# Kernel optimization log

Hardware: AMD Instinct MI355X
Metric: run time of the kernel (lower is better)

## Reference

```python
import jax, jax.numpy as jnp
import numpy as np

# Config: num_elems=64, num_attrs=8, vocab=1024, max_len=16, hidden=1024,
# input_embedding_dim=64, output_embedding_dim=256, num_layers=1, LSTM cell,
# attention=False, peeky=False, message=None, eval mode (argmax sampling).
B, A, NE = 2048, 8, 64
EIN, EOUT, H, V, L = 64, 256, 1024, 1024, 16


def setup_inputs() -> dict:
    key = jax.random.key(0)
    ks = jax.random.split(key, 12)
    s = 0.05
    return {
        "x": jax.random.randint(ks[0], (B, A), 0, NE),
        "in_emb": jax.random.normal(ks[1], (NE, EIN), jnp.float32) * s,
        "out_emb": jax.random.normal(ks[2], (V, EOUT), jnp.float32) * s,
        "W_in": jax.random.normal(ks[3], (H, A * EIN), jnp.float32) * s,
        "b_in": jnp.zeros((H,), jnp.float32),
        "W_ih": jax.random.normal(ks[4], (4 * H, EOUT), jnp.float32) * s,
        "b_ih": jnp.zeros((4 * H,), jnp.float32),
        "W_hh": jax.random.normal(ks[5], (4 * H, H), jnp.float32) * s,
        "b_hh": jnp.zeros((4 * H,), jnp.float32),
        "W_out": jax.random.normal(ks[6], (V, H), jnp.float32) * s,
        "b_out": jnp.zeros((V,), jnp.float32),
        "sos": jax.random.normal(ks[7], (EOUT,), jnp.float32),
    }


def reference(x, in_emb, out_emb, W_in, b_in, W_ih, b_ih, W_hh, b_hh, W_out, b_out, sos):
    bsz = x.shape[0]
    # input embedding -> concat attrs -> initial hidden
    ie = in_emb[x].reshape(bsz, -1)              # [B, A*EIN]
    h0 = ie @ W_in.T + b_in                      # [B, H]
    c0 = jnp.zeros_like(h0)                      # LSTM cell state starts at 0
    emb0 = jnp.broadcast_to(sos, (bsz, sos.shape[0]))  # SOS embedding [B, EOUT]

    def step(carry, _):
        h, c, emb = carry
        gates = emb @ W_ih.T + b_ih + h @ W_hh.T + b_hh  # [B, 4H], torch gate order i,f,g,o
        i, f, g, o = jnp.split(gates, 4, axis=-1)
        c_new = jax.nn.sigmoid(f) * c + jax.nn.sigmoid(i) * jnp.tanh(g)
        h_new = jax.nn.sigmoid(o) * jnp.tanh(c_new)
        logits = h_new @ W_out.T + b_out                 # [B, V]
        symbol = jnp.argmax(logits, axis=-1)             # eval-mode greedy sampling
        return (h_new, c_new, out_emb[symbol]), (symbol, logits)

    _, (syms, logits) = jax.lax.scan(step, (h0, c0, emb0), None, length=L)
    sequence = syms.T                                    # [B, L]
    logits = jnp.transpose(logits, (1, 0, 2))            # [B, L, V]
    return sequence, logits
```

## Files before the change

### kernel.cpp

```cpp
#include <hip/hip_runtime.h>
#include <math.h>

constexpr int kB    = 2048;
constexpr int kA    = 8;
constexpr int kEin  = 64;
constexpr int kEout = 256;
constexpr int kH    = 1024;
constexpr int kV    = 1024;
constexpr int kL    = 16;
constexpr int kKin  = kA * kEin;
constexpr int kNG   = 4 * kH;
constexpr float kInvLo = 1.0f / 2048.0f;

using half8 = __attribute__((ext_vector_type(8))) _Float16;
using half4 = __attribute__((ext_vector_type(4))) _Float16;
using f32x4 = __attribute__((ext_vector_type(4))) float;

#define GLL16(g, l) __builtin_amdgcn_global_load_lds(                        \
    (const __attribute__((address_space(1))) void*)(g),                      \
    (__attribute__((address_space(3))) void*)(l), 16, 0, 0)

__device__ __forceinline__ float sigm(float x) { return 1.0f / (1.0f + expf(-x)); }

struct HL { _Float16 hi, lo; };
__device__ __forceinline__ HL split2v(float x) {
  HL r;
  r.hi = (_Float16)x;
  r.lo = (_Float16)((x - (float)r.hi) * 2048.0f);
  return r;
}

__device__ __forceinline__ size_t packA(int m, int k) {
  return ((((size_t)(m >> 7) * 32 + (k >> 5)) * 4 + ((k >> 3) & 3)) * 128 + (m & 127)) * 8 + (k & 7);
}

__global__ __launch_bounds__(256) void init_state(float* __restrict__ c,
                                                  int* __restrict__ sym) {
  int i = blockIdx.x * 256 + threadIdx.x;
  c[i] = 0.0f;
  if (i < kB) sym[i] = kV;
}

__global__ __launch_bounds__(256) void split_plain(const float* __restrict__ src,
                                                   _Float16* __restrict__ hi,
                                                   _Float16* __restrict__ lo,
                                                   int n4) {
  int i = blockIdx.x * 256 + threadIdx.x;
  if (i >= n4) return;
  float4 v = ((const float4*)src)[i];
  half4 h, l;
  HL s0 = split2v(v.x), s1 = split2v(v.y), s2 = split2v(v.z), s3 = split2v(v.w);
  h.x = s0.hi; l.x = s0.lo; h.y = s1.hi; l.y = s1.lo;
  h.z = s2.hi; l.z = s2.lo; h.w = s3.hi; l.w = s3.lo;
  *(half4*)(hi + (size_t)i * 4) = h;
  *(half4*)(lo + (size_t)i * 4) = l;
}

__global__ __launch_bounds__(320) void split_gates_w(const float* __restrict__ W_ih,
                                                     const float* __restrict__ W_hh,
                                                     _Float16* __restrict__ rm_hi,
                                                     _Float16* __restrict__ rm_lo,
                                                     _Float16* __restrict__ p_hi,
                                                     _Float16* __restrict__ p_lo) {
  const int n  = blockIdx.x;
  const int k4 = threadIdx.x * 4;
  const int g  = (n >> 4) & 3;
  const int j  = ((n >> 6) << 4) | (n & 15);
  const int src = g * kH + j;
  float4 v = (k4 < kEout) ? *(const float4*)&W_ih[(size_t)src * kEout + k4]
                          : *(const float4*)&W_hh[(size_t)src * kH + (k4 - kEout)];
  half4 h, l;
  HL s0 = split2v(v.x), s1 = split2v(v.y), s2 = split2v(v.z), s3 = split2v(v.w);
  h.x = s0.hi; l.x = s0.lo; h.y = s1.hi; l.y = s1.lo;
  h.z = s2.hi; l.z = s2.lo; h.w = s3.hi; l.w = s3.lo;
  if (k4 < kEout) {
    *(half4*)(rm_hi + (size_t)n * kEout + k4) = h;
    *(half4*)(rm_lo + (size_t)n * kEout + k4) = l;
  } else {
    const int kp = k4 - kEout;
    const size_t ad = packA(n, kp);
    *(half4*)(p_hi + ad) = h;
    *(half4*)(p_lo + ad) = l;
  }
}

__global__ __launch_bounds__(256) void split_pack_wo(const float* __restrict__ W_out,
                                                     _Float16* __restrict__ hi,
                                                     _Float16* __restrict__ lo) {
  const int n  = blockIdx.x;
  const int k4 = threadIdx.x * 4;
  float4 v = *(const float4*)&W_out[(size_t)n * kH + k4];
  half4 h, l;
  HL s0 = split2v(v.x), s1 = split2v(v.y), s2 = split2v(v.z), s3 = split2v(v.w);
  h.x = s0.hi; l.x = s0.lo; h.y = s1.hi; l.y = s1.lo;
  h.z = s2.hi; l.z = s2.lo; h.w = s3.hi; l.w = s3.lo;
  const size_t ad = ((((size_t)(n >> 5) * 32 + (k4 >> 5)) * 4 + ((k4 >> 3) & 3)) * 32
                     + (n & 31)) * 8 + (k4 & 7);
  *(half4*)(hi + ad) = h;
  *(half4*)(lo + ad) = l;
}

__global__ __launch_bounds__(256) void h0_gemm(const int* __restrict__ x,
                                               const float* __restrict__ in_emb,
                                               const float* __restrict__ W_in,
                                               const float* __restrict__ b_in,
                                               _Float16* __restrict__ h_hi,
                                               _Float16* __restrict__ h_lo) {
  __shared__ float As[16][128];
  __shared__ float Bs[16][128];
  const int t  = threadIdx.x;
  const int tx = t & 15, ty = t >> 4;
  const int r  = t >> 1;
  const int kc = (t & 1) * 8;
  const int m0 = blockIdx.x * 128;
  const int n0 = blockIdx.y * 128;
  float acc[8][8] = {};
  for (int k0 = 0; k0 < kKin; k0 += 16) {
    const int kk   = k0 + kc;
    const int attr = kk >> 6;
    const int e    = kk & 63;
    const int idx  = x[(m0 + r) * kA + attr];
    const float* pa = in_emb + (size_t)idx * kEin + e;
    float4 a0 = *(const float4*)pa;
    float4 a1 = *(const float4*)(pa + 4);
    const float* pb = W_in + (size_t)(n0 + r) * kKin + kk;
    float4 b0 = *(const float4*)pb;
    float4 b1 = *(const float4*)(pb + 4);
    __syncthreads();
    As[kc+0][r]=a0.x; As[kc+1][r]=a0.y; As[kc+2][r]=a0.z; As[kc+3][r]=a0.w;
    As[kc+4][r]=a1.x; As[kc+5][r]=a1.y; As[kc+6][r]=a1.z; As[kc+7][r]=a1.w;
    Bs[kc+0][r]=b0.x; Bs[kc+1][r]=b0.y; Bs[kc+2][r]=b0.z; Bs[kc+3][r]=b0.w;
    Bs[kc+4][r]=b1.x; Bs[kc+5][r]=b1.y; Bs[kc+6][r]=b1.z; Bs[kc+7][r]=b1.w;
    __syncthreads();
#pragma unroll
    for (int k = 0; k < 16; ++k) {
      float a[8], b[8];
      *(float4*)&a[0] = *(const float4*)&As[k][ty*8];
      *(float4*)&a[4] = *(const float4*)&As[k][ty*8+4];
      *(float4*)&b[0] = *(const float4*)&Bs[k][tx*8];
      *(float4*)&b[4] = *(const float4*)&Bs[k][tx*8+4];
#pragma unroll
      for (int i = 0; i < 8; ++i)
#pragma unroll
        for (int j = 0; j < 8; ++j)
          acc[i][j] = fmaf(a[i], b[j], acc[i][j]);
    }
  }
#pragma unroll
  for (int i = 0; i < 8; ++i) {
    const int gm  = m0 + ty*8 + i;
    const int gn0 = n0 + tx*8;
    half8 h8, l8;
#pragma unroll
    for (int j = 0; j < 8; ++j) {
      HL s = split2v(acc[i][j] + b_in[gn0 + j]);
      h8[j] = s.hi; l8[j] = s.lo;
    }
    const size_t ad = packA(gm, gn0);
    *(half8*)(h_hi + ad) = h8;
    *(half8*)(h_lo + ad) = l8;
  }
}

__global__ __launch_bounds__(256, 2) void eg_gemm(
    const _Float16* __restrict__ oe_hi, const _Float16* __restrict__ oe_lo,
    const _Float16* __restrict__ Wg_hi, const _Float16* __restrict__ Wg_lo,
    float* __restrict__ Eg) {
  __shared__ __align__(16) _Float16 Ah[4][128][8], Al[4][128][8],
                                    Bh[4][128][8], Bl[4][128][8];
  const int t    = threadIdx.x;
  const int m0   = blockIdx.x * 128;
  const int by   = blockIdx.y;
  const int n0   = by * 128;
  const int r    = t & 127, q = t >> 7;
  const int rw   = r & 64;
  const int lane = t & 63, wid = t >> 6;
  const int wm   = (wid >> 1) * 64;
  const int wnv  = wid & 1;
  const int lc   = lane & 15, lg = lane >> 4;
  f32x4 acc1[4][4] = {}; f32x4 acc2[4][4] = {};
  for (int k0 = 0; k0 < kEout; k0 += 32) {
    const size_t oa = (size_t)(m0 + r) * kEout + k0 + q * 16;
    const size_t ob = (size_t)(n0 + r) * kEout + k0 + q * 16;
    __syncthreads();
    GLL16(oe_hi + oa,     &Ah[2*q  ][rw][0]);
    GLL16(oe_hi + oa + 8, &Ah[2*q+1][rw][0]);
    GLL16(oe_lo + oa,     &Al[2*q  ][rw][0]);
    GLL16(oe_lo + oa + 8, &Al[2*q+1][rw][0]);
    GLL16(Wg_hi + ob,     &Bh[2*q  ][rw][0]);
    GLL16(Wg_hi + ob + 8, &Bh[2*q+1][rw][0]);
    GLL16(Wg_lo + ob,     &Bl[2*q  ][rw][0]);
    GLL16(Wg_lo + ob + 8, &Bl[2*q+1][rw][0]);
    __syncthreads();
    half8 ah[4], al[4], bh[4], bl[4];
#pragma unroll
    for (int mf = 0; mf < 4; ++mf) {
      ah[mf] = *(const half8*)&Ah[lg][wm + mf*16 + lc][0];
      al[mf] = *(const half8*)&Al[lg][wm + mf*16 + lc][0];
    }
#pragma unroll
    for (int nf = 0; nf < 4; ++nf) {
      bh[nf] = *(const half8*)&Bh[lg][wnv*64 + nf*16 + lc][0];
      bl[nf] = *(const half8*)&Bl[lg][wnv*64 + nf*16 + lc][0];
    }
#pragma unroll
    for (int mf = 0; mf < 4; ++mf)
#pragma unroll
      for (int nf = 0; nf < 4; ++nf) {
        acc1[mf][nf] = __builtin_amdgcn_mfma_f32_16x16x32_f16(ah[mf], bh[nf], acc1[mf][nf], 0, 0, 0);
        acc2[mf][nf] = __builtin_amdgcn_mfma_f32_16x16x32_f16(ah[mf], bl[nf], acc2[mf][nf], 0, 0, 0);
        acc2[mf][nf] = __builtin_amdgcn_mfma_f32_16x16x32_f16(al[mf], bh[nf], acc2[mf][nf], 0, 0, 0);
      }
  }
#pragma unroll
  for (int mf = 0; mf < 4; ++mf)
#pragma unroll
    for (int reg = 0; reg < 4; ++reg) {
      const int m = m0 + wm + mf * 16 + lg * 4 + reg;
#pragma unroll
      for (int nf = 0; nf < 4; ++nf)
        Eg[(size_t)m * kNG + n0 + wnv*64 + nf*16 + lc] =
            acc1[mf][nf][reg] + acc2[mf][nf][reg] * kInvLo;
    }
}

__global__ __launch_bounds__(256) void gs_row(const float* __restrict__ sos,
                                              const float* __restrict__ W_ih,
                                              float* __restrict__ Eg) {
  const int n = blockIdx.x * 256 + threadIdx.x;
  const int g = (n >> 4) & 3;
  const int j = ((n >> 6) << 4) | (n & 15);
  const float* w = W_ih + (size_t)(g * kH + j) * kEout;
  float s = 0.0f;
#pragma unroll 4
  for (int k = 0; k < kEout; k += 4) {
    float4 wv = *(const float4*)&w[k];
    float4 sv = *(const float4*)&sos[k];
    s += wv.x*sv.x + wv.y*sv.y + wv.z*sv.z + wv.w*sv.w;
  }
  Eg[(size_t)kV * kNG + n] = s;
}

__global__ __launch_bounds__(256, 2) void gates_lstm_mfma(
    const _Float16* __restrict__ hp_hi,  const _Float16* __restrict__ hp_lo,
    const _Float16* __restrict__ Wgp_hi, const _Float16* __restrict__ Wgp_lo,
    const float* __restrict__ Eg,        const int* __restrict__ sym,
    const float* __restrict__ b_ih, const float* __restrict__ b_hh,
    float* __restrict__ c,
    _Float16* __restrict__ ho_hi, _Float16* __restrict__ ho_lo) {
  const int t    = threadIdx.x;
  const int bx   = blockIdx.x;
  const int by   = blockIdx.y;
  const int m0   = bx * 128;
  const int lane = t & 63, wid = t >> 6;
  const int wm   = (wid >> 1) * 64;
  const int wnv  = wid & 1;
  const int lc   = lane & 15, lg = lane >> 4;
  constexpr int SK = 4 * 128 * 8;

  size_t adr_a = (size_t)bx * 32 * SK + ((size_t)lg * 128 + wm + lc) * 8;
  size_t adr_b = (size_t)by * 32 * SK + ((size_t)lg * 128 + wnv * 64 + lc) * 8;

  f32x4 acc1[4][4] = {}; f32x4 acc2[4][4] = {};
  for (int ks = 0; ks < 32; ++ks) {
    half8 ah[4], al[4], bh[4], bl[4];
#pragma unroll
    for (int mf = 0; mf < 4; ++mf) {
      ah[mf] = *(const half8*)(hp_hi + adr_a + mf * 128);
      al[mf] = *(const half8*)(hp_lo + adr_a + mf * 128);
    }
#pragma unroll
    for (int nf = 0; nf < 4; ++nf) {
      bh[nf] = *(const half8*)(Wgp_hi + adr_b + nf * 128);
      bl[nf] = *(const half8*)(Wgp_lo + adr_b + nf * 128);
    }
#pragma unroll
    for (int mf = 0; mf < 4; ++mf)
#pragma unroll
      for (int nf = 0; nf < 4; ++nf) {
        acc1[mf][nf] = __builtin_amdgcn_mfma_f32_16x16x32_f16(ah[mf], bh[nf], acc1[mf][nf], 0, 0, 0);
        acc2[mf][nf] = __builtin_amdgcn_mfma_f32_16x16x32_f16(ah[mf], bl[nf], acc2[mf][nf], 0, 0, 0);
        acc2[mf][nf] = __builtin_amdgcn_mfma_f32_16x16x32_f16(al[mf], bh[nf], acc2[mf][nf], 0, 0, 0);
      }
    adr_a += SK; adr_b += SK;
  }
  const int j   = by * 32 + wnv * 16 + lc;
  const int nbase = by * 128 + wnv * 64 + lc;
  const int jks = j >> 5, jq = (j >> 3) & 3, je = j & 7;
  float bb[4];
#pragma unroll
  for (int nf = 0; nf < 4; ++nf) bb[nf] = b_ih[nf * kH + j] + b_hh[nf * kH + j];
#pragma unroll
  for (int mf = 0; mf < 4; ++mf)
#pragma unroll
    for (int reg = 0; reg < 4; ++reg) {
      const int lr = wm + mf * 16 + lg * 4 + reg;
      const int m  = m0 + lr;
      const size_t off = (size_t)m * kH + j;
      const float* Erow = Eg + (size_t)sym[m] * kNG + nbase;
      const float vi = acc1[mf][0][reg] + acc2[mf][0][reg] * kInvLo + bb[0] + Erow[0];
      const float vf = acc1[mf][1][reg] + acc2[mf][1][reg] * kInvLo + bb[1] + Erow[16];
      const float vg = acc1[mf][2][reg] + acc2[mf][2][reg] * kInvLo + bb[2] + Erow[32];
      const float vo = acc1[mf][3][reg] + acc2[mf][3][reg] * kInvLo + bb[3] + Erow[48];
      const float cn = sigm(vf) * c[off] + sigm(vi) * tanhf(vg);
      const float hn = sigm(vo) * tanhf(cn);
      c[off] = cn;
      HL s = split2v(hn);
      const size_t ad = ((((size_t)bx * 32 + jks) * 4 + jq) * 128 + lr) * 8 + je;
      ho_hi[ad] = s.hi; ho_lo[ad] = s.lo;
    }
}

__global__ __launch_bounds__(256, 2) void logits_mfma(
    const _Float16* __restrict__ hp_hi, const _Float16* __restrict__ hp_lo,
    const _Float16* __restrict__ Wop_hi, const _Float16* __restrict__ Wop_lo,
    const float* __restrict__ b_out, float* __restrict__ out) {
  const int t    = threadIdx.x;
  const int bx   = blockIdx.x;
  const int by   = blockIdx.y;
  const int lane = t & 63, wid = t >> 6;
  const int wm   = wid * 32;
  const int lc   = lane & 15, lg = lane >> 4;
  constexpr int SKA = 4 * 128 * 8;
  constexpr int SKB = 4 * 32 * 8;

  size_t adr_a = (size_t)bx * 32 * SKA + ((size_t)lg * 128 + wm + lc) * 8;
  size_t adr_b = (size_t)by * 32 * SKB + ((size_t)lg * 32 + lc) * 8;

  f32x4 acc1[2][2] = {}; f32x4 acc2[2][2] = {};
#pragma unroll 2
  for (int ks = 0; ks < 32; ++ks) {
    half8 ah[2], al[2], bh[2], bl[2];
#pragma unroll
    for (int mf = 0; mf < 2; ++mf) {
      ah[mf] = *(const half8*)(hp_hi + adr_a + mf * 128);
      al[mf] = *(const half8*)(hp_lo + adr_a + mf * 128);
    }
#pragma unroll
    for (int nf = 0; nf < 2; ++nf) {
      bh[nf] = *(const half8*)(Wop_hi + adr_b + nf * 128);
      bl[nf] = *(const half8*)(Wop_lo + adr_b + nf * 128);
    }
#pragma unroll
    for (int mf = 0; mf < 2; ++mf)
#pragma unroll
      for (int nf = 0; nf < 2; ++nf) {
        acc1[mf][nf] = __builtin_amdgcn_mfma_f32_16x16x32_f16(ah[mf], bh[nf], acc1[mf][nf], 0, 0, 0);
        acc2[mf][nf] = __builtin_amdgcn_mfma_f32_16x16x32_f16(ah[mf], bl[nf], acc2[mf][nf], 0, 0, 0);
        acc2[mf][nf] = __builtin_amdgcn_mfma_f32_16x16x32_f16(al[mf], bh[nf], acc2[mf][nf], 0, 0, 0);
      }
    adr_a += SKA; adr_b += SKB;
  }
#pragma unroll
  for (int mf = 0; mf < 2; ++mf)
#pragma unroll
    for (int reg = 0; reg < 4; ++reg) {
      const int m = bx * 128 + wm + mf * 16 + lg * 4 + reg;
#pragma unroll
      for (int nf = 0; nf < 2; ++nf) {
        const int n = by * 32 + nf * 16 + lc;
        out[(size_t)m * (kL * kV) + n] = acc1[mf][nf][reg] + acc2[mf][nf][reg] * kInvLo + b_out[n];
      }
    }
}

__global__ __launch_bounds__(256) void argmax_gather(const float* __restrict__ logits_t,
                                                     float* __restrict__ seq,
                                                     int* __restrict__ sym,
                                                     int t) {
  const int lane = threadIdx.x & 63;
  const int wv   = threadIdx.x >> 6;
  const int b    = blockIdx.x * 4 + wv;
  const float* row = logits_t + (size_t)b * (kL * kV);
  float m = -3.4e38f;
  int  mi = 0;
#pragma unroll
  for (int jr = 0; jr < kV / 64; ++jr) {
    const int idx = jr * 64 + lane;
    const float v = row[idx];
    if (v > m) { m = v; mi = idx; }
  }
#pragma unroll
  for (int off = 32; off > 0; off >>= 1) {
    const float om = __shfl_down(m, off);
    const int   oi = __shfl_down(mi, off);
    if (om > m || (om == m && oi < mi)) { m = om; mi = oi; }
  }
  if (lane == 0) {
    seq[(size_t)b * kL + t] = (float)mi;
    sym[b] = mi;
  }
}

extern "C" void kernel_launch(void* const* d_in, const int* in_sizes, int n_in,
                              void* d_out, int out_size, void* d_ws, size_t ws_size,
                              hipStream_t stream) {
  const int*   x       = (const int*)d_in[0];
  const float* in_emb  = (const float*)d_in[1];
  const float* out_emb = (const float*)d_in[2];
  const float* W_in    = (const float*)d_in[3];
  const float* b_in    = (const float*)d_in[4];
  const float* W_ih    = (const float*)d_in[5];
  const float* b_ih    = (const float*)d_in[6];
  const float* W_hh    = (const float*)d_in[7];
  const float* b_hh    = (const float*)d_in[8];
  const float* W_out   = (const float*)d_in[9];
  const float* b_out   = (const float*)d_in[10];
  const float* sos     = (const float*)d_in[11];

  float* cb  = (float*)d_ws;
  float* Eg  = cb + (size_t)kB * kH;
  int*   sym = (int*)(Eg + (size_t)(kV + 1) * kNG);
  _Float16* hp = (_Float16*)(sym + kB);
  const size_t nBH = (size_t)kB * kH;
  _Float16* hA_hi  = hp;            _Float16* hA_lo  = hp + nBH;
  _Float16* hB_hi  = hp + 2*nBH;    _Float16* hB_lo  = hp + 3*nBH;
  _Float16* Wgrm_hi = hp + 4*nBH;
  _Float16* Wgrm_lo = Wgrm_hi + (size_t)kNG*kEout;
  _Float16* Wgp_hi  = Wgrm_lo + (size_t)kNG*kEout;
  _Float16* Wgp_lo  = Wgp_hi + (size_t)kNG*kH;
  _Float16* Wop_hi  = Wgp_lo + (size_t)kNG*kH;
  _Float16* Wop_lo  = Wop_hi + (size_t)kV*kH;
  _Float16* oe_hi   = Wop_lo + (size_t)kV*kH;
  _Float16* oe_lo   = oe_hi + (size_t)kV*kEout;

  float* seq    = (float*)d_out;
  float* logits = seq + (size_t)kB * kL;

  init_state<<<(kB * kH) / 256, 256, 0, stream>>>(cb, sym);
  split_gates_w<<<kNG, 320, 0, stream>>>(W_ih, W_hh, Wgrm_hi, Wgrm_lo, Wgp_hi, Wgp_lo);
  split_pack_wo<<<kV, 256, 0, stream>>>(W_out, Wop_hi, Wop_lo);
  split_plain<<<(kV * kEout / 4) / 256, 256, 0, stream>>>(out_emb, oe_hi, oe_lo, kV * kEout / 4);
  eg_gemm<<<dim3(kV / 128, kNG / 128), 256, 0, stream>>>(oe_hi, oe_lo, Wgrm_hi, Wgrm_lo, Eg);
  gs_row<<<kNG / 256, 256, 0, stream>>>(sos, W_ih, Eg);
  h0_gemm<<<dim3(kB / 128, kH / 128), 256, 0, stream>>>(x, in_emb, W_in, b_in, hA_hi, hA_lo);

  for (int t = 0; t < kL; ++t) {
    const _Float16* hi_h = (t & 1) ? hB_hi : hA_hi;
    const _Float16* hi_l = (t & 1) ? hB_lo : hA_lo;
    _Float16* ho_h = (t & 1) ? hA_hi : hB_hi;
    _Float16* ho_l = (t & 1) ? hA_lo : hB_lo;
    gates_lstm_mfma<<<dim3(kB / 128, kNG / 128), 256, 0, stream>>>(
        hi_h, hi_l, Wgp_hi, Wgp_lo, Eg, sym, b_ih, b_hh, cb, ho_h, ho_l);
    logits_mfma<<<dim3(kB / 128, kV / 32), 256, 0, stream>>>(
        ho_h, ho_l, Wop_hi, Wop_lo, b_out, logits + (size_t)t * kV);
    argmax_gather<<<kB / 4, 256, 0, stream>>>(logits + (size_t)t * kV, seq, sym, t);
  }
}
```

Measured before the change: 1.813 ms.

## Fuse argmax into logits GEMM via atomic keys; move h0 GEMM to MFMA

The separate argmax kernel is removed. Each logits block reduces its 32 columns and atomically maxes a packed 64-bit (value, index) key into a per-step key array, and the next gates kernel decodes the symbol and writes the sequence entry. The fp32 h0 GEMM is replaced by prepacked split-fp16 operands and an MFMA kernel. This saves one launch per step and a re-read of the logits, at the cost of global 64-bit atomics and extra packing kernels.

```diff
diff --git a/kernel.cpp b/kernel.cpp
--- a/kernel.cpp
+++ b/kernel.cpp
@@ -15,6 +15,7 @@
 using half8 = __attribute__((ext_vector_type(8))) _Float16;
 using half4 = __attribute__((ext_vector_type(4))) _Float16;
 using f32x4 = __attribute__((ext_vector_type(4))) float;
+using u64   = unsigned long long;
 
 #define GLL16(g, l) __builtin_amdgcn_global_load_lds(                        \
     (const __attribute__((address_space(1))) void*)(g),                      \
@@ -30,15 +31,24 @@
   return r;
 }
 
-__device__ __forceinline__ size_t packA(int m, int k) {
-  return ((((size_t)(m >> 7) * 32 + (k >> 5)) * 4 + ((k >> 3) & 3)) * 128 + (m & 127)) * 8 + (k & 7);
+__device__ __forceinline__ size_t packAK(int m, int k, int nks) {
+  return ((((size_t)(m >> 7) * nks + (k >> 5)) * 4 + ((k >> 3) & 3)) * 128 + (m & 127)) * 8 + (k & 7);
+}
+
+__device__ __forceinline__ u64 amax_key(float v, int idx) {
+  unsigned b = __float_as_uint(v);
+  unsigned u = (b & 0x80000000u) ? ~b : (b | 0x80000000u);
+  return ((u64)u << 10) | (unsigned)(1023 - idx);
+}
+__device__ __forceinline__ int key_sym(u64 k) {
+  return k == 0 ? kV : 1023 - (int)(k & 1023);
 }
 
 __global__ __launch_bounds__(256) void init_state(float* __restrict__ c,
-                                                  int* __restrict__ sym) {
+                                                  u64* __restrict__ keys) {
   int i = blockIdx.x * 256 + threadIdx.x;
   c[i] = 0.0f;
-  if (i < kB) sym[i] = kV;
+  if (i < 17 * kB) keys[i] = 0ull;
 }
 
 __global__ __launch_bounds__(256) void split_plain(const float* __restrict__ src,
@@ -77,8 +87,7 @@
     *(half4*)(rm_hi + (size_t)n * kEout + k4) = h;
     *(half4*)(rm_lo + (size_t)n * kEout + k4) = l;
   } else {
-    const int kp = k4 - kEout;
-    const size_t ad = packA(n, kp);
+    const size_t ad = packAK(n, k4 - kEout, 32);
     *(half4*)(p_hi + ad) = h;
     *(half4*)(p_lo + ad) = l;
   }
@@ -100,66 +109,91 @@
   *(half4*)(lo + ad) = l;
 }
 
-__global__ __launch_bounds__(256) void h0_gemm(const int* __restrict__ x,
+__global__ __launch_bounds__(128) void pack_a0(const int* __restrict__ x,
                                                const float* __restrict__ in_emb,
-                                               const float* __restrict__ W_in,
-                                               const float* __restrict__ b_in,
-                                               _Float16* __restrict__ h_hi,
-                                               _Float16* __restrict__ h_lo) {
-  __shared__ float As[16][128];
-  __shared__ float Bs[16][128];
-  const int t  = threadIdx.x;
-  const int tx = t & 15, ty = t >> 4;
-  const int r  = t >> 1;
-  const int kc = (t & 1) * 8;
-  const int m0 = blockIdx.x * 128;
-  const int n0 = blockIdx.y * 128;
-  float acc[8][8] = {};
-  for (int k0 = 0; k0 < kKin; k0 += 16) {
-    const int kk   = k0 + kc;
-    const int attr = kk >> 6;
-    const int e    = kk & 63;
-    const int idx  = x[(m0 + r) * kA + attr];
-    const float* pa = in_emb + (size_t)idx * kEin + e;
-    float4 a0 = *(const float4*)pa;
-    float4 a1 = *(const float4*)(pa + 4);
-    const float* pb = W_in + (size_t)(n0 + r) * kKin + kk;
-    float4 b0 = *(const float4*)pb;
-    float4 b1 = *(const float4*)(pb + 4);
-    __syncthreads();
-    As[kc+0][r]=a0.x; As[kc+1][r]=a0.y; As[kc+2][r]=a0.z; As[kc+3][r]=a0.w;
-    As[kc+4][r]=a1.x; As[kc+5][r]=a1.y; As[kc+6][r]=a1.z; As[kc+7][r]=a1.w;
-    Bs[kc+0][r]=b0.x; Bs[kc+1][r]=b0.y; Bs[kc+2][r]=b0.z; Bs[kc+3][r]=b0.w;
-    Bs[kc+4][r]=b1.x; Bs[kc+5][r]=b1.y; Bs[kc+6][r]=b1.z; Bs[kc+7][r]=b1.w;
-    __syncthreads();
-#pragma unroll
-    for (int k = 0; k < 16; ++k) {
-      float a[8], b[8];
-      *(float4*)&a[0] = *(const float4*)&As[k][ty*8];
-      *(float4*)&a[4] = *(const float4*)&As[k][ty*8+4];
-      *(float4*)&b[0] = *(const float4*)&Bs[k][tx*8];
-      *(float4*)&b[4] = *(const float4*)&Bs[k][tx*8+4];
-#pragma unroll
-      for (int i = 0; i < 8; ++i)
-#pragma unroll
-        for (int j = 0; j < 8; ++j)
-          acc[i][j] = fmaf(a[i], b[j], acc[i][j]);
-    }
-  }
-#pragma unroll
-  for (int i = 0; i < 8; ++i) {
-    const int gm  = m0 + ty*8 + i;
-    const int gn0 = n0 + tx*8;
-    half8 h8, l8;
-#pragma unroll
-    for (int j = 0; j < 8; ++j) {
-      HL s = split2v(acc[i][j] + b_in[gn0 + j]);
-      h8[j] = s.hi; l8[j] = s.lo;
-    }
-    const size_t ad = packA(gm, gn0);
-    *(half8*)(h_hi + ad) = h8;
-    *(half8*)(h_lo + ad) = l8;
-  }
+                                               _Float16* __restrict__ hi,
+                                               _Float16* __restrict__ lo) {
+  const int m  = blockIdx.x;
+  const int k4 = threadIdx.x * 4;
+  const int idx = x[m * kA + (k4 >> 6)];
+  float4 v = *(const float4*)&in_emb[(size_t)idx * kEin + (k4 & 63)];
+  half4 h, l;
+  HL s0 = split2v(v.x), s1 = split2v(v.y), s2 = split2v(v.z), s3 = split2v(v.w);
+  h.x = s0.hi; l.x = s0.lo; h.y = s1.hi; l.y = s1.lo;
+  h.z = s2.hi; l.z = s2.lo; h.w = s3.hi; l.w = s3.lo;
+  const size_t ad = packAK(m, k4, 16);
+  *(half4*)(hi + ad) = h;
+  *(half4*)(lo + ad) = l;
+}
+
+__global__ __launch_bounds__(128) void pack_w0(const float* __restrict__ W_in,
+                                               _Float16* __restrict__ hi,
+                                               _Float16* __restrict__ lo) {
+  const int n  = blockIdx.x;
+  const int k4 = threadIdx.x * 4;
+  float4 v = *(const float4*)&W_in[(size_t)n * kKin + k4];
+  half4 h, l;
+  HL s0 = split2v(v.x), s1 = split2v(v.y), s2 = split2v(v.z), s3 = split2v(v.w);
+  h.x = s0.hi; l.x = s0.lo; h.y = s1.hi; l.y = s1.lo;
+  h.z = s2.hi; l.z = s2.lo; h.w = s3.hi; l.w = s3.lo;
+  const size_t ad = packAK(n, k4, 16);
+  *(half4*)(hi + ad) = h;
+  *(half4*)(lo + ad) = l;
+}
+
+__global__ __launch_bounds__(256, 2) void h0_mfma(
+    const _Float16* __restrict__ a_hi, const _Float16* __restrict__ a_lo,
+    const _Float16* __restrict__ w_hi, const _Float16* __restrict__ w_lo,
+    const float* __restrict__ b_in,
+    _Float16* __restrict__ h_hi, _Float16* __restrict__ h_lo) {
+  const int t    = threadIdx.x;
+  const int bx   = blockIdx.x;
+  const int by   = blockIdx.y;
+  const int lane = t & 63, wid = t >> 6;
+  const int wm   = (wid >> 1) * 64;
+  const int wnv  = wid & 1;
+  const int lc   = lane & 15, lg = lane >> 4;
+  constexpr int SK = 4 * 128 * 8;
+
+  size_t adr_a = (size_t)bx * 16 * SK + ((size_t)lg * 128 + wm + lc) * 8;
+  size_t adr_b = (size_t)by * 16 * SK + ((size_t)lg * 128 + wnv * 64 + lc) * 8;
+
+  f32x4 acc1[4][4] = {}; f32x4 acc2[4][4] = {};
+  for (int ks = 0; ks < 16; ++ks) {
+    half8 ah[4], al[4], bh[4], bl[4];
+#pragma unroll
+    for (int mf = 0; mf < 4; ++mf) {
+      ah[mf] = *(const half8*)(a_hi + adr_a + mf * 128);
+      al[mf] = *(const half8*)(a_lo + adr_a + mf * 128);
+    }
+#pragma unroll
+    for (int nf = 0; nf < 4; ++nf) {
+      bh[nf] = *(const half8*)(w_hi + adr_b + nf * 128);
+      bl[nf] = *(const half8*)(w_lo + adr_b + nf * 128);
+    }
+#pragma unroll
+    for (int mf = 0; mf < 4; ++mf)
+#pragma unroll
+      for (int nf = 0; nf < 4; ++nf) {
+        acc1[mf][nf] = __builtin_amdgcn_mfma_f32_16x16x32_f16(ah[mf], bh[nf], acc1[mf][nf], 0, 0, 0);
+        acc2[mf][nf] = __builtin_amdgcn_mfma_f32_16x16x32_f16(ah[mf], bl[nf], acc2[mf][nf], 0, 0, 0);
+        acc2[mf][nf] = __builtin_amdgcn_mfma_f32_16x16x32_f16(al[mf], bh[nf], acc2[mf][nf], 0, 0, 0);
+      }
+    adr_a += SK; adr_b += SK;
+  }
+#pragma unroll
+  for (int mf = 0; mf < 4; ++mf)
+#pragma unroll
+    for (int reg = 0; reg < 4; ++reg) {
+      const int gm = bx * 128 + wm + mf * 16 + lg * 4 + reg;
+#pragma unroll
+      for (int nf = 0; nf < 4; ++nf) {
+        const int j = by * 128 + wnv * 64 + nf * 16 + lc;
+        HL s = split2v(acc1[mf][nf][reg] + acc2[mf][nf][reg] * kInvLo + b_in[j]);
+        const size_t ad = packAK(gm, j, 32);
+        h_hi[ad] = s.hi; h_lo[ad] = s.lo;
+      }
+    }
 }
 
 __global__ __launch_bounds__(256, 2) void eg_gemm(
@@ -244,15 +278,16 @@
 __global__ __launch_bounds__(256, 2) void gates_lstm_mfma(
     const _Float16* __restrict__ hp_hi,  const _Float16* __restrict__ hp_lo,
     const _Float16* __restrict__ Wgp_hi, const _Float16* __restrict__ Wgp_lo,
-    const float* __restrict__ Eg,        const int* __restrict__ sym,
+    const float* __restrict__ Eg,        const u64* __restrict__ keys,
     const float* __restrict__ b_ih, const float* __restrict__ b_hh,
     float* __restrict__ c,
-    _Float16* __restrict__ ho_hi, _Float16* __restrict__ ho_lo) {
-  const int t    = threadIdx.x;
+    _Float16* __restrict__ ho_hi, _Float16* __restrict__ ho_lo,
+    float* __restrict__ seq, int t) {
+  const int tid  = threadIdx.x;
   const int bx   = blockIdx.x;
   const int by   = blockIdx.y;
   const int m0   = bx * 128;
-  const int lane = t & 63, wid = t >> 6;
+  const int lane = tid & 63, wid = tid >> 6;
   const int wm   = (wid >> 1) * 64;
   const int wnv  = wid & 1;
   const int lc   = lane & 15, lg = lane >> 4;
@@ -297,7 +332,10 @@
       const int lr = wm + mf * 16 + lg * 4 + reg;
       const int m  = m0 + lr;
       const size_t off = (size_t)m * kH + j;
-      const float* Erow = Eg + (size_t)sym[m] * kNG + nbase;
+      const int s = key_sym(keys[m]);
+      if (by == 0 && wnv == 0 && lc == 0 && t > 0)
+        seq[(size_t)m * kL + (t - 1)] = (float)(s);
+      const float* Erow = Eg + (size_t)s * kNG + nbase;
       const float vi = acc1[mf][0][reg] + acc2[mf][0][reg] * kInvLo + bb[0] + Erow[0];
       const float vf = acc1[mf][1][reg] + acc2[mf][1][reg] * kInvLo + bb[1] + Erow[16];
       const float vg = acc1[mf][2][reg] + acc2[mf][2][reg] * kInvLo + bb[2] + Erow[32];
@@ -305,16 +343,17 @@
       const float cn = sigm(vf) * c[off] + sigm(vi) * tanhf(vg);
       const float hn = sigm(vo) * tanhf(cn);
       c[off] = cn;
-      HL s = split2v(hn);
+      HL sp = split2v(hn);
       const size_t ad = ((((size_t)bx * 32 + jks) * 4 + jq) * 128 + lr) * 8 + je;
-      ho_hi[ad] = s.hi; ho_lo[ad] = s.lo;
+      ho_hi[ad] = sp.hi; ho_lo[ad] = sp.lo;
     }
 }
 
 __global__ __launch_bounds__(256, 2) void logits_mfma(
     const _Float16* __restrict__ hp_hi, const _Float16* __restrict__ hp_lo,
     const _Float16* __restrict__ Wop_hi, const _Float16* __restrict__ Wop_lo,
-    const float* __restrict__ b_out, float* __restrict__ out) {
+    const float* __restrict__ b_out, float* __restrict__ out,
+    u64* __restrict__ keys) {
   const int t    = threadIdx.x;
   const int bx   = blockIdx.x;
   const int by   = blockIdx.y;
@@ -356,40 +395,31 @@
 #pragma unroll
     for (int reg = 0; reg < 4; ++reg) {
       const int m = bx * 128 + wm + mf * 16 + lg * 4 + reg;
+      float v[2];
 #pragma unroll
       for (int nf = 0; nf < 2; ++nf) {
         const int n = by * 32 + nf * 16 + lc;
-        out[(size_t)m * (kL * kV) + n] = acc1[mf][nf][reg] + acc2[mf][nf][reg] * kInvLo + b_out[n];
-      }
-    }
-}
-
-__global__ __launch_bounds__(256) void argmax_gather(const float* __restrict__ logits_t,
-                                                     float* __restrict__ seq,
-                                                     int* __restrict__ sym,
-                                                     int t) {
-  const int lane = threadIdx.x & 63;
-  const int wv   = threadIdx.x >> 6;
-  const int b    = blockIdx.x * 4 + wv;
-  const float* row = logits_t + (size_t)b * (kL * kV);
-  float m = -3.4e38f;
-  int  mi = 0;
-#pragma unroll
-  for (int jr = 0; jr < kV / 64; ++jr) {
-    const int idx = jr * 64 + lane;
-    const float v = row[idx];
-    if (v > m) { m = v; mi = idx; }
-  }
-#pragma unroll
-  for (int off = 32; off > 0; off >>= 1) {
-    const float om = __shfl_down(m, off);
-    const int   oi = __shfl_down(mi, off);
-    if (om > m || (om == m && oi < mi)) { m = om; mi = oi; }
-  }
-  if (lane == 0) {
-    seq[(size_t)b * kL + t] = (float)mi;
-    sym[b] = mi;
-  }
+        v[nf] = acc1[mf][nf][reg] + acc2[mf][nf][reg] * kInvLo + b_out[n];
+        out[(size_t)m * (kL * kV) + n] = v[nf];
+      }
+      float bv = v[0]; int bi = by * 32 + lc;
+      if (v[1] > bv) { bv = v[1]; bi = by * 32 + 16 + lc; }
+#pragma unroll
+      for (int off = 1; off < 16; off <<= 1) {
+        const float ov = __shfl_xor(bv, off);
+        const int   oi = __shfl_xor(bi, off);
+        if (ov > bv || (ov == bv && oi < bi)) { bv = ov; bi = oi; }
+      }
+      if (lc == 0) atomicMax(&keys[m], amax_key(bv, bi));
+    }
+}
+
+__global__ __launch_bounds__(256) void final_decode(const u64* __restrict__ keys,
+                                                    float* __restrict__ seq) {
+  const int b = blockIdx.x * 256 + threadIdx.x;
+  if (b >= kB) return;
+  const u64 k = keys[b];
+  seq[(size_t)b * kL + (kL - 1)] = (float)(k == 0 ? 0 : 1023 - (int)(k & 1023));
 }
 
 extern "C" void kernel_launch(void* const* d_in, const int* in_sizes, int n_in,
@@ -410,8 +440,8 @@
 
   float* cb  = (float*)d_ws;
   float* Eg  = cb + (size_t)kB * kH;
-  int*   sym = (int*)(Eg + (size_t)(kV + 1) * kNG);
-  _Float16* hp = (_Float16*)(sym + kB);
+  u64*  keys = (u64*)(Eg + (size_t)(kV + 1) * kNG);
+  _Float16* hp = (_Float16*)(keys + 17 * (size_t)kB);
   const size_t nBH = (size_t)kB * kH;
   _Float16* hA_hi  = hp;            _Float16* hA_lo  = hp + nBH;
   _Float16* hB_hi  = hp + 2*nBH;    _Float16* hB_lo  = hp + 3*nBH;
@@ -423,17 +453,23 @@
   _Float16* Wop_lo  = Wop_hi + (size_t)kV*kH;
   _Float16* oe_hi   = Wop_lo + (size_t)kV*kH;
   _Float16* oe_lo   = oe_hi + (size_t)kV*kEout;
+  _Float16* A0_hi   = oe_lo + (size_t)kV*kEout;
+  _Float16* A0_lo   = A0_hi + (size_t)kB*kKin;
+  _Float16* W0_hi   = A0_lo + (size_t)kB*kKin;
+  _Float16* W0_lo   = W0_hi + (size_t)kH*kKin;
 
   float* seq    = (float*)d_out;
   float* logits = seq + (size_t)kB * kL;
 
-  init_state<<<(kB * kH) / 256, 256, 0, stream>>>(cb, sym);
+  init_state<<<(kB * kH) / 256, 256, 0, stream>>>(cb, keys);
   split_gates_w<<<kNG, 320, 0, stream>>>(W_ih, W_hh, Wgrm_hi, Wgrm_lo, Wgp_hi, Wgp_lo);
   split_pack_wo<<<kV, 256, 0, stream>>>(W_out, Wop_hi, Wop_lo);
   split_plain<<<(kV * kEout / 4) / 256, 256, 0, stream>>>(out_emb, oe_hi, oe_lo, kV * kEout / 4);
+  pack_a0<<<kB, 128, 0, stream>>>(x, in_emb, A0_hi, A0_lo);
+  pack_w0<<<kH, 128, 0, stream>>>(W_in, W0_hi, W0_lo);
   eg_gemm<<<dim3(kV / 128, kNG / 128), 256, 0, stream>>>(oe_hi, oe_lo, Wgrm_hi, Wgrm_lo, Eg);
   gs_row<<<kNG / 256, 256, 0, stream>>>(sos, W_ih, Eg);
-  h0_gemm<<<dim3(kB / 128, kH / 128), 256, 0, stream>>>(x, in_emb, W_in, b_in, hA_hi, hA_lo);
+  h0_mfma<<<dim3(kB / 128, kH / 128), 256, 0, stream>>>(A0_hi, A0_lo, W0_hi, W0_lo, b_in, hA_hi, hA_lo);
 
   for (int t = 0; t < kL; ++t) {
     const _Float16* hi_h = (t & 1) ? hB_hi : hA_hi;
@@ -441,9 +477,11 @@
     _Float16* ho_h = (t & 1) ? hA_hi : hB_hi;
     _Float16* ho_l = (t & 1) ? hA_lo : hB_lo;
     gates_lstm_mfma<<<dim3(kB / 128, kNG / 128), 256, 0, stream>>>(
-        hi_h, hi_l, Wgp_hi, Wgp_lo, Eg, sym, b_ih, b_hh, cb, ho_h, ho_l);
+        hi_h, hi_l, Wgp_hi, Wgp_lo, Eg, keys + (size_t)t * kB,
+        b_ih, b_hh, cb, ho_h, ho_l, seq, t);
     logits_mfma<<<dim3(kB / 128, kV / 32), 256, 0, stream>>>(
-        ho_h, ho_l, Wop_hi, Wop_lo, b_out, logits + (size_t)t * kV);
-    argmax_gather<<<kB / 4, 256, 0, stream>>>(logits + (size_t)t * kV, seq, sym, t);
-  }
-}
+        ho_h, ho_l, Wop_hi, Wop_lo, b_out, logits + (size_t)t * kV,
+        keys + (size_t)(t + 1) * kB);
+  }
+  final_decode<<<kB / 256, 256, 0, stream>>>(keys + 16 * (size_t)kB, seq);
+}
```

Result: faster. 1.771 ms (-2.3%).
